# Optimization experiments

Measured on AMD Instinct MI355X. Metric: run time of the kernel, lower is better.

## Reference

```python
import jax, jax.numpy as jnp
import numpy as np

NEG_PENALTY = 0.03
B, C_TOTAL, C_LOADED = 2048, 1000, 256


def setup_inputs() -> dict:
    key = jax.random.key(0)
    k1, k2, k3 = jax.random.split(key, 3)
    ranks = jax.random.normal(k1, (B, C_TOTAL), dtype=jnp.float32)
    labels = jax.random.randint(k2, (B, C_TOTAL), 0, 2, dtype=jnp.int32)
    class_ids_loaded = jnp.sort(jax.random.randint(k3, (C_LOADED,), 0, C_TOTAL, dtype=jnp.int64))
    return {"ranks": ranks, "labels": labels, "class_ids_loaded": class_ids_loaded}


def reference(ranks, labels, class_ids_loaded):
    # Select loaded classes: [B, C]
    lab = labels[:, class_ids_loaded].astype(ranks.dtype)
    r = ranks[:, class_ids_loaded]
    pos = lab            # 1 where label == 1 (correct)
    neg = 1.0 - lab      # 1 where label == 0 (wrong)
    # Pairwise hinge: relu(penalty + wrong_rank - correct_rank) over all (correct p, wrong n) pairs.
    # pen[b, p, n] = relu(NEG_PENALTY + r[b, n] - r[b, p]); mask after relu == computing only valid pairs.
    pen = jax.nn.relu(NEG_PENALTY + r[:, None, :] - r[:, :, None])  # [B, C, C]
    total = jnp.einsum('bpn,bp,bn->', pen, pos, neg)
    # Denominator: number of rows with at least one positive label.
    n_valid = jnp.sum(jnp.any(lab == 1.0, axis=1)).astype(ranks.dtype)
    return (total / n_valid).reshape((1,))
```

## Files before the change

kernel.cpp:

```cpp
#include <hip/hip_runtime.h>

#define B_ROWS 2048
#define C_TOTAL 1000
#define C_LOADED 256
#define NEG_PEN 0.03f
#define NLINES 64


union PVU { unsigned long long u; float2 f; };

__global__ void __launch_bounds__(C_LOADED)
rank_loss_fused(const float* __restrict__ ranks,
                const int* __restrict__ labels,
                const int* __restrict__ ids,
                unsigned long long* __restrict__ pv,
                unsigned int* __restrict__ lines,
                unsigned int* __restrict__ lvl2,
                float* __restrict__ out) {
    __shared__ __align__(16) float negl[264];
    __shared__ float posl[256];
    __shared__ float wave_sums[4];
    __shared__ int wb_n[4], wb_p[4];
    __shared__ int ncnt, pcnt, finflag;
    __shared__ float red_s[4], red_v[4];

    const int b = blockIdx.x;
    const int t = threadIdx.x;
    const int lane = t & 63;
    const int wave = t >> 6;

    if (t == 0) { ncnt = 0; pcnt = 0; finflag = 0; }

    const int c = ids[t];
    const float r = ranks[b * C_TOTAL + c];
    const int lab = labels[b * C_TOTAL + c];
    const bool isneg = (lab == 0);

    const unsigned long long m = __ballot(isneg);
    const unsigned long long lm = (1ULL << lane) - 1ULL;
    const int nneg_w = __popcll(m);
    const int my_n = __popcll(m & lm);
    const int my_p = __popcll(~m & lm);

    __syncthreads();
    if (lane == 0) {
        wb_n[wave] = atomicAdd(&ncnt, nneg_w);
        wb_p[wave] = atomicAdd(&pcnt, 64 - nneg_w);
    }
    __syncthreads();

    const int N = ncnt;
    const int P = C_LOADED - N;
    const int Npad = (N + 7) & ~7;
    if (isneg) negl[wb_n[wave] + my_n] = r + NEG_PEN;
    else       posl[wb_p[wave] + my_p] = r;
    if (t >= N && t < Npad) negl[t] = -1e30f;
    __syncthreads();

    float acc = 0.f;
    if (t < P) {
        const float rp = posl[t];
        float a0 = 0.f, a1 = 0.f, a2 = 0.f, a3 = 0.f;
        float a4 = 0.f, a5 = 0.f, a6 = 0.f, a7 = 0.f;
        const float4* n4 = (const float4*)negl;
        const int G = Npad >> 2;
        for (int g = 0; g < G; g += 2) {
            float4 x = n4[g];
            float4 y = n4[g + 1];
            a0 += fmaxf(x.x - rp, 0.0f);
            a1 += fmaxf(x.y - rp, 0.0f);
            a2 += fmaxf(x.z - rp, 0.0f);
            a3 += fmaxf(x.w - rp, 0.0f);
            a4 += fmaxf(y.x - rp, 0.0f);
            a5 += fmaxf(y.y - rp, 0.0f);
            a6 += fmaxf(y.z - rp, 0.0f);
            a7 += fmaxf(y.w - rp, 0.0f);
        }
        acc = ((a0 + a1) + (a2 + a3)) + ((a4 + a5) + (a6 + a7));
    }

#pragma unroll
    for (int off = 32; off > 0; off >>= 1) {
        acc += __shfl_down(acc, off, 64);
    }
    if (lane == 0) wave_sums[wave] = acc;
    __syncthreads();

    if (t == 0) {
        PVU v;
        v.f = make_float2(
            (wave_sums[0] + wave_sums[1]) + (wave_sums[2] + wave_sums[3]),
            (P > 0) ? 1.0f : 0.0f);
        (void)__hip_atomic_exchange(&pv[b], v.u, __ATOMIC_RELAXED,
                                    __HIP_MEMORY_SCOPE_AGENT);
        asm volatile("s_waitcnt vmcnt(0)" ::: "memory");
        unsigned int v1 = __hip_atomic_fetch_add(&lines[(b & (NLINES - 1)) * 16],
                                                 1u, __ATOMIC_RELAXED,
                                                 __HIP_MEMORY_SCOPE_AGENT);
        if ((v1 & 31u) == 31u) {
            unsigned int v2 = __hip_atomic_fetch_add(lvl2, 1u, __ATOMIC_RELAXED,
                                                     __HIP_MEMORY_SCOPE_AGENT);
            if ((v2 & 63u) == 63u) finflag = 1;
        }
    }
    __syncthreads();

    if (finflag) {
        float ssum = 0.f, svld = 0.f;
#pragma unroll
        for (int k = 0; k < 8; ++k) {
            PVU v;
            v.u = __hip_atomic_load(&pv[t * 8 + k], __ATOMIC_RELAXED,
                                    __HIP_MEMORY_SCOPE_AGENT);
            ssum += v.f.x;
            svld += v.f.y;
        }
#pragma unroll
        for (int off = 32; off > 0; off >>= 1) {
            ssum += __shfl_down(ssum, off, 64);
            svld += __shfl_down(svld, off, 64);
        }
        if (lane == 0) { red_s[wave] = ssum; red_v[wave] = svld; }
        __syncthreads();
        if (t == 0) {
            float ts = (red_s[0] + red_s[1]) + (red_s[2] + red_s[3]);
            float tv = (red_v[0] + red_v[1]) + (red_v[2] + red_v[3]);
            out[0] = ts / tv;
        }
    }
}

extern "C" void kernel_launch(void* const* d_in, const int* in_sizes, int n_in,
                              void* d_out, int out_size, void* d_ws, size_t ws_size,
                              hipStream_t stream) {
    const float* ranks  = (const float*)d_in[0];
    const int*   labels = (const int*)d_in[1];
    const int*   ids    = (const int*)d_in[2];
    float* out = (float*)d_out;

    unsigned long long* pv = (unsigned long long*)d_ws;
    unsigned int* lines = (unsigned int*)((char*)d_ws + 16384);
    unsigned int* lvl2  = (unsigned int*)((char*)d_ws + 20480);

    rank_loss_fused<<<B_ROWS, C_LOADED, 0, stream>>>(ranks, labels, ids,
                                                     pv, lines, lvl2, out);
}
```

Measured before the change: 12.12 us.

## Map one row per wavefront and drop block-level barriers

Each 64-lane wavefront now handles a whole row, with four rows per 256-thread block. Every lane holds up to four positives and loops over the negatives, which removes the __syncthreads barriers and shared-memory atomics used for compaction. The completion counter and final reduction become per-wave, and the last wave reads all 2048 partials itself. The trade-off is a longer serial loop per lane (up to four positives times N negatives) and divergent template dispatch, in exchange for less synchronisation and fewer blocks.

New measurement: 11.95 us. No clear change (-1.3%).

```diff
diff --git a/kernel.cpp b/kernel.cpp
--- a/kernel.cpp
+++ b/kernel.cpp
@@ -5,11 +5,33 @@
 #define C_LOADED 256
 #define NEG_PEN 0.03f
 #define NLINES 64
+#define WPB 4
+#define GRID (B_ROWS / WPB)
 
 
 union PVU { unsigned long long u; float2 f; };
 
-__global__ void __launch_bounds__(C_LOADED)
+template<int QMAX>
+__device__ __forceinline__ float pair_loop(const float4* __restrict__ n4, int G,
+                                           float rp0, float rp1,
+                                           float rp2, float rp3) {
+    float a0 = 0.f, a1 = 0.f, a2 = 0.f, a3 = 0.f;
+    for (int g = 0; g < G; g += 2) {
+        float4 x = n4[g];
+        float4 y = n4[g + 1];
+        float v[8] = {x.x, x.y, x.z, x.w, y.x, y.y, y.z, y.w};
+#pragma unroll
+        for (int e = 0; e < 8; ++e) {
+            a0 += fmaxf(v[e] - rp0, 0.f);
+            if (QMAX > 1) a1 += fmaxf(v[e] - rp1, 0.f);
+            if (QMAX > 2) a2 += fmaxf(v[e] - rp2, 0.f);
+            if (QMAX > 3) a3 += fmaxf(v[e] - rp3, 0.f);
+        }
+    }
+    return (a0 + a1) + (a2 + a3);
+}
+
+__global__ void __launch_bounds__(256)
 rank_loss_fused(const float* __restrict__ ranks,
                 const int* __restrict__ labels,
                 const int* __restrict__ ids,
@@ -17,116 +39,109 @@
                 unsigned int* __restrict__ lines,
                 unsigned int* __restrict__ lvl2,
                 float* __restrict__ out) {
-    __shared__ __align__(16) float negl[264];
-    __shared__ float posl[256];
-    __shared__ float wave_sums[4];
-    __shared__ int wb_n[4], wb_p[4];
-    __shared__ int ncnt, pcnt, finflag;
-    __shared__ float red_s[4], red_v[4];
+    __shared__ __align__(16) float negl[WPB][264];
+    __shared__ __align__(16) float posl[WPB][256];
 
-    const int b = blockIdx.x;
     const int t = threadIdx.x;
     const int lane = t & 63;
     const int wave = t >> 6;
+    const int row = blockIdx.x * WPB + wave;
 
-    if (t == 0) { ncnt = 0; pcnt = 0; finflag = 0; }
+    const int c0 = ids[lane];
+    const int c1 = ids[lane + 64];
+    const int c2 = ids[lane + 128];
+    const int c3 = ids[lane + 192];
+    const int base = row * C_TOTAL;
+    const float r0 = ranks[base + c0], r1 = ranks[base + c1];
+    const float r2 = ranks[base + c2], r3 = ranks[base + c3];
+    const int l0 = labels[base + c0], l1 = labels[base + c1];
+    const int l2 = labels[base + c2], l3 = labels[base + c3];
 
-    const int c = ids[t];
-    const float r = ranks[b * C_TOTAL + c];
-    const int lab = labels[b * C_TOTAL + c];
-    const bool isneg = (lab == 0);
+    const unsigned long long m0 = __ballot(l0 == 0);
+    const unsigned long long m1 = __ballot(l1 == 0);
+    const unsigned long long m2 = __ballot(l2 == 0);
+    const unsigned long long m3 = __ballot(l3 == 0);
+    const int n0 = __popcll(m0), n1 = __popcll(m1);
+    const int n2 = __popcll(m2), n3 = __popcll(m3);
+    const int N = n0 + n1 + n2 + n3;
+    const int P = C_LOADED - N;
+    const unsigned long long lm = (1ULL << lane) - 1ULL;
 
-    const unsigned long long m = __ballot(isneg);
-    const unsigned long long lm = (1ULL << lane) - 1ULL;
-    const int nneg_w = __popcll(m);
-    const int my_n = __popcll(m & lm);
-    const int my_p = __popcll(~m & lm);
+    float* ng = negl[wave];
+    float* ps = posl[wave];
+    const int nb1 = n0, nb2 = n0 + n1, nb3 = n0 + n1 + n2;
+    const int pb1 = 64 - n0, pb2 = 128 - nb2, pb3 = 192 - nb3;
+    if (l0 == 0) ng[__popcll(m0 & lm)] = r0 + NEG_PEN;
+    else         ps[__popcll(~m0 & lm)] = r0;
+    if (l1 == 0) ng[nb1 + __popcll(m1 & lm)] = r1 + NEG_PEN;
+    else         ps[pb1 + __popcll(~m1 & lm)] = r1;
+    if (l2 == 0) ng[nb2 + __popcll(m2 & lm)] = r2 + NEG_PEN;
+    else         ps[pb2 + __popcll(~m2 & lm)] = r2;
+    if (l3 == 0) ng[nb3 + __popcll(m3 & lm)] = r3 + NEG_PEN;
+    else         ps[pb3 + __popcll(~m3 & lm)] = r3;
 
-    __syncthreads();
-    if (lane == 0) {
-        wb_n[wave] = atomicAdd(&ncnt, nneg_w);
-        wb_p[wave] = atomicAdd(&pcnt, 64 - nneg_w);
-    }
-    __syncthreads();
+    const int Npad = (N + 7) & ~7;
+    if (lane < Npad - N) ng[N + lane] = -1e30f;
 
-    const int N = ncnt;
-    const int P = C_LOADED - N;
-    const int Npad = (N + 7) & ~7;
-    if (isneg) negl[wb_n[wave] + my_n] = r + NEG_PEN;
-    else       posl[wb_p[wave] + my_p] = r;
-    if (t >= N && t < Npad) negl[t] = -1e30f;
-    __syncthreads();
+    asm volatile("s_waitcnt lgkmcnt(0)" ::: "memory");
 
     float acc = 0.f;
-    if (t < P) {
-        const float rp = posl[t];
-        float a0 = 0.f, a1 = 0.f, a2 = 0.f, a3 = 0.f;
-        float a4 = 0.f, a5 = 0.f, a6 = 0.f, a7 = 0.f;
-        const float4* n4 = (const float4*)negl;
+    if (P > 0) {
+        const int qmax = (P + 63) >> 6;
+        float rp0 = 3e30f, rp1 = 3e30f, rp2 = 3e30f, rp3 = 3e30f;
+        if (lane < P)       rp0 = ps[lane];
+        if (lane + 64 < P)  rp1 = ps[lane + 64];
+        if (lane + 128 < P) rp2 = ps[lane + 128];
+        if (lane + 192 < P) rp3 = ps[lane + 192];
+        const float4* n4 = (const float4*)ng;
         const int G = Npad >> 2;
-        for (int g = 0; g < G; g += 2) {
-            float4 x = n4[g];
-            float4 y = n4[g + 1];
-            a0 += fmaxf(x.x - rp, 0.0f);
-            a1 += fmaxf(x.y - rp, 0.0f);
-            a2 += fmaxf(x.z - rp, 0.0f);
-            a3 += fmaxf(x.w - rp, 0.0f);
-            a4 += fmaxf(y.x - rp, 0.0f);
-            a5 += fmaxf(y.y - rp, 0.0f);
-            a6 += fmaxf(y.z - rp, 0.0f);
-            a7 += fmaxf(y.w - rp, 0.0f);
+        switch (qmax) {
+        case 1:  acc = pair_loop<1>(n4, G, rp0, rp1, rp2, rp3); break;
+        case 2:  acc = pair_loop<2>(n4, G, rp0, rp1, rp2, rp3); break;
+        case 3:  acc = pair_loop<3>(n4, G, rp0, rp1, rp2, rp3); break;
+        default: acc = pair_loop<4>(n4, G, rp0, rp1, rp2, rp3); break;
         }
-        acc = ((a0 + a1) + (a2 + a3)) + ((a4 + a5) + (a6 + a7));
     }
 
 #pragma unroll
     for (int off = 32; off > 0; off >>= 1) {
         acc += __shfl_down(acc, off, 64);
     }
-    if (lane == 0) wave_sums[wave] = acc;
-    __syncthreads();
 
-    if (t == 0) {
+    int fin = 0;
+    if (lane == 0) {
         PVU v;
-        v.f = make_float2(
-            (wave_sums[0] + wave_sums[1]) + (wave_sums[2] + wave_sums[3]),
-            (P > 0) ? 1.0f : 0.0f);
-        (void)__hip_atomic_exchange(&pv[b], v.u, __ATOMIC_RELAXED,
+        v.f = make_float2(acc, (P > 0) ? 1.0f : 0.0f);
+        (void)__hip_atomic_exchange(&pv[row], v.u, __ATOMIC_RELAXED,
                                     __HIP_MEMORY_SCOPE_AGENT);
         asm volatile("s_waitcnt vmcnt(0)" ::: "memory");
-        unsigned int v1 = __hip_atomic_fetch_add(&lines[(b & (NLINES - 1)) * 16],
-                                                 1u, __ATOMIC_RELAXED,
-                                                 __HIP_MEMORY_SCOPE_AGENT);
+        unsigned int v1 = __hip_atomic_fetch_add(
+            &lines[(row & (NLINES - 1)) * 16], 1u,
+            __ATOMIC_RELAXED, __HIP_MEMORY_SCOPE_AGENT);
         if ((v1 & 31u) == 31u) {
-            unsigned int v2 = __hip_atomic_fetch_add(lvl2, 1u, __ATOMIC_RELAXED,
-                                                     __HIP_MEMORY_SCOPE_AGENT);
-            if ((v2 & 63u) == 63u) finflag = 1;
+            unsigned int v2 = __hip_atomic_fetch_add(
+                lvl2, 1u, __ATOMIC_RELAXED, __HIP_MEMORY_SCOPE_AGENT);
+            if ((v2 & 63u) == 63u) fin = 1;
         }
     }
-    __syncthreads();
+    fin = __shfl(fin, 0, 64);
 
-    if (finflag) {
-        float ssum = 0.f, svld = 0.f;
+    if (fin) {
+        float ss = 0.f, sv = 0.f;
 #pragma unroll
-        for (int k = 0; k < 8; ++k) {
+        for (int k = 0; k < 32; ++k) {
             PVU v;
-            v.u = __hip_atomic_load(&pv[t * 8 + k], __ATOMIC_RELAXED,
+            v.u = __hip_atomic_load(&pv[k * 64 + lane], __ATOMIC_RELAXED,
                                     __HIP_MEMORY_SCOPE_AGENT);
-            ssum += v.f.x;
-            svld += v.f.y;
+            ss += v.f.x;
+            sv += v.f.y;
         }
 #pragma unroll
         for (int off = 32; off > 0; off >>= 1) {
-            ssum += __shfl_down(ssum, off, 64);
-            svld += __shfl_down(svld, off, 64);
+            ss += __shfl_down(ss, off, 64);
+            sv += __shfl_down(sv, off, 64);
         }
-        if (lane == 0) { red_s[wave] = ssum; red_v[wave] = svld; }
-        __syncthreads();
-        if (t == 0) {
-            float ts = (red_s[0] + red_s[1]) + (red_s[2] + red_s[3]);
-            float tv = (red_v[0] + red_v[1]) + (red_v[2] + red_v[3]);
-            out[0] = ts / tv;
-        }
+        if (lane == 0) out[0] = ss / sv;
     }
 }
 
@@ -142,6 +157,6 @@
     unsigned int* lines = (unsigned int*)((char*)d_ws + 16384);
     unsigned int* lvl2  = (unsigned int*)((char*)d_ws + 20480);
 
-    rank_loss_fused<<<B_ROWS, C_LOADED, 0, stream>>>(ranks, labels, ids,
-                                                     pv, lines, lvl2, out);
+    rank_loss_fused<<<GRID, 256, 0, stream>>>(ranks, labels, ids,
+                                              pv, lines, lvl2, out);
 }
```
